# Kernel tuning notes

Measured on AMD Instinct MI355X. Metric: run time of the kernel, lower is better.

The kernel has to match this reference:

```python
import jax, jax.numpy as jnp
import numpy as np

# dimensions
B, NQ, D, H, L, KT, KF = 4, 8192, 256, 8, 4, 2, 2
K = KT * KF
DH = D // H
SPATIAL = np.array([[64, 64], [32, 32], [16, 16], [8, 8]], dtype=np.int32)  # (H_l, W_l)
_sizes = SPATIAL[:, 0] * SPATIAL[:, 1]
LSI = np.concatenate([[0], np.cumsum(_sizes)[:-1]]).astype(np.int32)
NV = int(_sizes.sum())


def setup_inputs() -> dict:
    key = jax.random.key(0)
    ks = jax.random.split(key, 12)
    s = 0.02  # small weight scale keeps tanh in linear region like the zero-init original
    # biases per _reset_parameters: +-0.5 grid for offsets, level-specialization for level_weights
    b_time = jnp.asarray(np.tile(np.linspace(-0.5, 0.5, KT), H * L).astype(np.float32))
    b_freq = jnp.asarray(np.tile(np.linspace(-0.5, 0.5, KF).astype(np.float32), H * L))
    lvl_bias = np.zeros((H, L), dtype=np.float32)
    hpl = max(1, H // L)
    for lvl in range(L):
        lvl_bias[lvl * hpl:min(lvl * hpl + hpl, H), lvl] = 1.0
    return dict(
        query=jax.random.normal(ks[0], (B, NQ, D), jnp.float32),
        reference_points=jax.random.uniform(ks[1], (B, NQ, L, 2), jnp.float32),
        value=jax.random.normal(ks[2], (B, NV, D), jnp.float32),
        spatial_shapes=jnp.asarray(SPATIAL),
        level_start_index=jnp.asarray(LSI),
        W_time=jax.random.normal(ks[3], (D, H * L * KT), jnp.float32) * s,
        b_time=b_time,
        W_freq=jax.random.normal(ks[4], (D, H * L * KF), jnp.float32) * s,
        b_freq=b_freq,
        W_lvl=jax.random.normal(ks[5], (D, H * L), jnp.float32) * s,
        b_lvl=jnp.asarray(lvl_bias.reshape(-1)),
        W_pt=jax.random.normal(ks[6], (D, H * L * K), jnp.float32) * s,
        b_pt=jnp.zeros((H * L * K,), jnp.float32),
        W_v=jax.random.normal(ks[7], (D, D), jnp.float32) * (1.0 / np.sqrt(D)),
        b_v=jnp.zeros((D,), jnp.float32),
        W_o=jax.random.normal(ks[8], (D, D), jnp.float32) * (1.0 / np.sqrt(D)),
        b_o=jnp.zeros((D,), jnp.float32),
    )


def _bilinear(vlev, gx, gy, Hl, Wl):
    # vlev: [B,H,Hl*Wl,DH]; gx,gy: [B,H,NQ,K] normalized grid coords in [-1,1]
    # F.grid_sample(align_corners=False, padding_mode='zeros') semantics
    x = (gx + 1.0) * (Wl * 0.5) - 0.5
    y = (gy + 1.0) * (Hl * 0.5) - 0.5
    x0 = jnp.floor(x)
    y0 = jnp.floor(y)
    wx1 = x - x0
    wy1 = y - y0
    x0i = x0.astype(jnp.int32)
    y0i = y0.astype(jnp.int32)

    def gather(xi, yi, w):
        valid = (xi >= 0) & (xi < Wl) & (yi >= 0) & (yi < Hl)
        idx = jnp.clip(yi, 0, Hl - 1) * Wl + jnp.clip(xi, 0, Wl - 1)
        b, h, nq, k = idx.shape
        v = jnp.take_along_axis(vlev, idx.reshape(b, h, nq * k)[..., None], axis=2)
        v = v.reshape(b, h, nq, k, DH)
        return v * (w * valid)[..., None]

    return (gather(x0i, y0i, (1.0 - wx1) * (1.0 - wy1))
            + gather(x0i + 1, y0i, wx1 * (1.0 - wy1))
            + gather(x0i, y0i + 1, (1.0 - wx1) * wy1)
            + gather(x0i + 1, y0i + 1, wx1 * wy1))


def _forward(query, reference_points, value, W_time, b_time, W_freq, b_freq,
             W_lvl, b_lvl, W_pt, b_pt, W_v, b_v, W_o, b_o,
             spatial_shapes, level_start_index):
    ss = np.asarray(spatial_shapes)
    lsi = np.asarray(level_start_index)
    # predicted separable offsets (offset_scale = 1.0)
    t_off = jnp.tanh(query @ W_time + b_time).reshape(B, NQ, H, L, KT)
    f_off = jnp.tanh(query @ W_freq + b_freq).reshape(B, NQ, H, L, KF)
    # square grid: outer product of time (x) and freq (y) offsets -> K = KT*KF points
    off = jnp.stack([
        jnp.broadcast_to(t_off[..., :, None], (B, NQ, H, L, KT, KF)),
        jnp.broadcast_to(f_off[..., None, :], (B, NQ, H, L, KT, KF)),
    ], axis=-1).reshape(B, NQ, H, L, K, 2)
    # normalizer: (W_l, H_l) per level
    norm = jnp.stack([spatial_shapes[:, 1], spatial_shapes[:, 0]], axis=-1).astype(jnp.float32)
    loc = reference_points[:, :, None, :, None, :] + off / norm[None, None, None, :, None, :]
    loc = jnp.clip(loc, 0.0, 1.0)
    grid = 2.0 * loc - 1.0  # [B,NQ,H,L,K,2], last dim = (x, y)
    # attention weights: softmax over levels times softmax over points
    lw = jax.nn.softmax((query @ W_lvl + b_lvl).reshape(B, NQ, H, L), axis=-1)
    pw = jax.nn.softmax((query @ W_pt + b_pt).reshape(B, NQ, H, L, K), axis=-1)
    attn = lw[..., None] * pw  # [B,NQ,H,L,K]
    v = (value @ W_v + b_v).reshape(B, NV, H, DH)
    out = jnp.zeros((B, NQ, H, DH), jnp.float32)
    for lid in range(L):
        Hl, Wl = int(ss[lid, 0]), int(ss[lid, 1])
        start = int(lsi[lid])
        vlev = v[:, start:start + Hl * Wl].transpose(0, 2, 1, 3)  # [B,H,S_l,DH]
        gx = grid[:, :, :, lid, :, 0].transpose(0, 2, 1, 3)  # [B,H,NQ,K]
        gy = grid[:, :, :, lid, :, 1].transpose(0, 2, 1, 3)
        sampled = _bilinear(vlev, gx, gy, Hl, Wl)  # [B,H,NQ,K,DH]
        a = attn[:, :, :, lid, :].transpose(0, 2, 1, 3)  # [B,H,NQ,K]
        out = out + jnp.einsum('bhqkd,bhqk->bqhd', sampled, a)
    out = out.reshape(B, NQ, D)
    return out @ W_o + b_o


def reference(query, reference_points, value, spatial_shapes, level_start_index,
              W_time, b_time, W_freq, b_freq, W_lvl, b_lvl, W_pt, b_pt,
              W_v, b_v, W_o, b_o):
    return _forward(query, reference_points, value, W_time, b_time, W_freq, b_freq,
                    W_lvl, b_lvl, W_pt, b_pt, W_v, b_v, W_o, b_o,
                    spatial_shapes, level_start_index)
```

## Files before the change

### kernel.cpp

```cpp
#include <hip/hip_runtime.h>
#include <math.h>

#define B_  4
#define NQ_ 8192
#define D_  256
#define H_  8
#define L_  4
#define K_  4
#define DH_ 32
#define NV_ 5440

#define SLAB_ 5936

typedef short bf16x8 __attribute__((ext_vector_type(8)));
typedef float f32x4  __attribute__((ext_vector_type(4)));
typedef float f32x8  __attribute__((ext_vector_type(8)));
typedef unsigned short u16x8 __attribute__((ext_vector_type(8)));

__device__ __forceinline__ ushort f2bf(float f) {
    union { float f; unsigned u; } v; v.f = f;
    return (ushort)((v.u + 0x7FFF + ((v.u >> 16) & 1)) >> 16);
}
__device__ __forceinline__ float bf2f(ushort u) {
    union { unsigned u; float f; } v; v.u = ((unsigned)u) << 16;
    return v.f;
}
__device__ __forceinline__ void gld16(const void* g, void* l) {
    __builtin_amdgcn_global_load_lds(
        (const __attribute__((address_space(1))) unsigned int*)g,
        (__attribute__((address_space(3))) unsigned int*)l, 16, 0, 0);
}

__global__ __launch_bounds__(256) void k_prep(const float* __restrict__ Wv,
                                              const float* __restrict__ Wo,
                                              const float* __restrict__ Wt,
                                              const float* __restrict__ Wf,
                                              const float* __restrict__ Wlv,
                                              const float* __restrict__ Wp,
                                              ushort* __restrict__ Wvt,
                                              ushort* __restrict__ Wot,
                                              ushort* __restrict__ Wqt) {
    const int bk = blockIdx.x;
    const int t  = threadIdx.x;
    if (bk < 512) {
        const float* in; ushort* out; int n;
        if (bk < 256) { in = Wv; out = Wvt; n = bk; }
        else          { in = Wo; out = Wot; n = bk - 256; }
        out[n * 256 + t] = f2bf(in[t * 256 + n]);
    } else {
        const int n = bk - 512;
        float v;
        if (n < 64)       v = Wt[t * 64 + n];
        else if (n < 128) v = Wf[t * 64 + (n - 64)];
        else if (n < 160) v = Wlv[t * 32 + (n - 128)];
        else              v = Wp[t * 128 + (n - 160)];
        Wqt[n * 256 + t] = f2bf(v);
    }
}

__device__ __forceinline__ void vproj_role(char* smem, int fid,
                                           const float* __restrict__ value,
                                           const ushort* __restrict__ Wvt,
                                           const float* __restrict__ bv,
                                           ushort* __restrict__ vperm) {
    ushort* As0 = (ushort*)smem;
    ushort* Bs0 = (ushort*)(smem + 16384);
    const int m0   = (fid % 170) * 128;
    const int n0   = (fid / 170) * 128;
    const int t    = threadIdx.x;
    const int w    = t >> 6;
    const int lane = t & 63;
    const int wm   = (w >> 1) * 64;
    const int wn   = (w & 1) * 64;
    const int lm   = lane & 15;
    const int quad = lane >> 4;

    float4 areg[4];

    auto stageB = [&](int buf, int kc) {
        ushort* B = Bs0 + buf * 4096;
        #pragma unroll
        for (int i = 0; i < 2; ++i) {
            const int c0 = (i * 4 + w) * 64;
            const int c  = c0 + lane;
            const int row = c >> 2, ko = (c & 3) * 8;
            gld16(&Wvt[(size_t)(n0 + row) * 256 + kc + ko], B + (size_t)c0 * 8);
        }
    };
    auto loadA = [&](int kc) {
        #pragma unroll
        for (int i = 0; i < 4; ++i) {
            const int c = t + i * 256;
            const int row = c >> 3, ko = (c & 7) * 4;
            areg[i] = *(const float4*)&value[(size_t)(m0 + row) * 256 + kc + ko];
        }
    };
    auto writeA = [&](int buf) {
        ushort* A = As0 + buf * 4096;
        #pragma unroll
        for (int i = 0; i < 4; ++i) {
            const int c = t + i * 256;
            const int row = c >> 3, ko = (c & 7) * 4;
            ushort4 u;
            u.x = f2bf(areg[i].x); u.y = f2bf(areg[i].y);
            u.z = f2bf(areg[i].z); u.w = f2bf(areg[i].w);
            *(ushort4*)&A[row * 32 + ko] = u;
        }
    };

    f32x4 acc[4][4];
    #pragma unroll
    for (int i = 0; i < 4; ++i)
        #pragma unroll
        for (int j = 0; j < 4; ++j)
            acc[i][j] = (f32x4)(0.f);

    loadA(0); writeA(0);
    stageB(0, 0);
    __syncthreads();

    int cur = 0;
    for (int kc = 0; kc < 256; kc += 32) {
        const int nxt = cur ^ 1;
        const ushort* Ac = As0 + cur * 4096;
        const ushort* Bc = Bs0 + cur * 4096;
        bf16x8 af[4], bfr[4];
        #pragma unroll
        for (int mf = 0; mf < 4; ++mf)
            af[mf] = *(const bf16x8*)&Ac[(wm + mf * 16 + lm) * 32 + quad * 8];
        #pragma unroll
        for (int nf = 0; nf < 4; ++nf)
            bfr[nf] = *(const bf16x8*)&Bc[(wn + nf * 16 + lm) * 32 + quad * 8];
        if (kc + 32 < 256) {
            loadA(kc + 32);
            stageB(nxt, kc + 32);
        }
        #pragma unroll
        for (int mf = 0; mf < 4; ++mf)
            #pragma unroll
            for (int nf = 0; nf < 4; ++nf)
                acc[mf][nf] = __builtin_amdgcn_mfma_f32_16x16x32_bf16(
                    af[mf], bfr[nf], acc[mf][nf], 0, 0, 0);
        if (kc + 32 < 256) {
            writeA(nxt);
            __syncthreads();
        }
        cur = nxt;
    }

    #pragma unroll
    for (int mf = 0; mf < 4; ++mf) {
        #pragma unroll
        for (int nf = 0; nf < 4; ++nf) {
            const f32x4 a = acc[mf][nf];
            const int col   = n0 + wn + nf * 16 + lm;
            const int rbase = m0 + wm + mf * 16 + quad * 4;
            #pragma unroll
            for (int r = 0; r < 4; ++r) {
                const int row = rbase + r;
                const float v = a[r];
                const int b = row / NV_, s = row - b * NV_;
                const int h = col >> 5, dh = col & 31;
                const int l = (s >= 5376) ? 3 : (s >= 5120) ? 2 : (s >= 4096) ? 1 : 0;
                const int lsi_[4] = {0, 4096, 5120, 5376};
                const int po_[4]  = {0, 4356, 5512, 5836};
                const int o  = s - lsi_[l];
                const int Wl = 64 >> l;
                const int y  = o >> (6 - l);
                const int x  = o & (Wl - 1);
                const int prow = po_[l] + (y + 1) * (Wl + 2) + (x + 1);
                vperm[(((size_t)(b * H_ + h)) * SLAB_ + prow) * 32 + dh] =
                    f2bf(v + bv[col]);
            }
        }
    }
}

__device__ __forceinline__ void qproj_role(char* smem, int fid,
                                           const float* __restrict__ query,
                                           const ushort* __restrict__ Wqt,
                                           const float* __restrict__ refpts,
                                           const float* __restrict__ bt,
                                           const float* __restrict__ bfq,
                                           const float* __restrict__ blv,
                                           const float* __restrict__ bp,
                                           float* __restrict__ params) {
    ushort* As0 = (ushort*)smem;
    ushort* Bs0 = (ushort*)(smem + 8192);
    float*  ep  = (float*)smem;

    const int m0   = fid * 64;
    const int t    = threadIdx.x;
    const int w    = t >> 6;
    const int lane = t & 63;
    const int wm   = (w >> 1) * 32;
    const int wn   = (w & 1) * 144;
    const int lm   = lane & 15;
    const int quad = lane >> 4;

    float4 areg[2];

    auto stageB = [&](int buf, int kc) {
        ushort* B = Bs0 + buf * 9216;
        #pragma unroll
        for (int i = 0; i < 5; ++i) {
            const int cb = i * 4 + w;
            if (cb < 18) {
                const int c0 = cb * 64;
                const int c  = c0 + lane;
                const int row = c >> 2, ko = (c & 3) * 8;
                gld16(&Wqt[(size_t)row * 256 + kc + ko], B + (size_t)c0 * 8);
            }
        }
    };
    auto loadA = [&](int kc) {
        #pragma unroll
        for (int i = 0; i < 2; ++i) {
            const int c = t + i * 256;
            const int row = c >> 3, ko = (c & 7) * 4;
            areg[i] = *(const float4*)&query[(size_t)(m0 + row) * 256 + kc + ko];
        }
    };
    auto writeA = [&](int buf) {
        ushort* A = As0 + buf * 2048;
        #pragma unroll
        for (int i = 0; i < 2; ++i) {
            const int c = t + i * 256;
            const int row = c >> 3, ko = (c & 7) * 4;
            ushort4 u;
            u.x = f2bf(areg[i].x); u.y = f2bf(areg[i].y);
            u.z = f2bf(areg[i].z); u.w = f2bf(areg[i].w);
            *(ushort4*)&A[row * 32 + ko] = u;
        }
    };

    f32x4 acc[2][9];
    #pragma unroll
    for (int i = 0; i < 2; ++i)
        #pragma unroll
        for (int j = 0; j < 9; ++j)
            acc[i][j] = (f32x4)(0.f);

    loadA(0); writeA(0);
    stageB(0, 0);
    __syncthreads();

    int cur = 0;
    for (int kc = 0; kc < 256; kc += 32) {
        const int nxt = cur ^ 1;
        const ushort* Ac = As0 + cur * 2048;
        const ushort* Bc = Bs0 + cur * 9216;
        bf16x8 af[2], bfr[9];
        #pragma unroll
        for (int mf = 0; mf < 2; ++mf)
            af[mf] = *(const bf16x8*)&Ac[(wm + mf * 16 + lm) * 32 + quad * 8];
        #pragma unroll
        for (int nf = 0; nf < 9; ++nf)
            bfr[nf] = *(const bf16x8*)&Bc[(wn + nf * 16 + lm) * 32 + quad * 8];
        if (kc + 32 < 256) {
            loadA(kc + 32);
            stageB(nxt, kc + 32);
        }
        #pragma unroll
        for (int mf = 0; mf < 2; ++mf)
            #pragma unroll
            for (int nf = 0; nf < 9; ++nf)
                acc[mf][nf] = __builtin_amdgcn_mfma_f32_16x16x32_bf16(
                    af[mf], bfr[nf], acc[mf][nf], 0, 0, 0);
        if (kc + 32 < 256) {
            writeA(nxt);
            __syncthreads();
        }
        cur = nxt;
    }

    #pragma unroll
    for (int ph = 0; ph < 2; ++ph) {
        __syncthreads();
        if ((w >> 1) == ph) {
            #pragma unroll
            for (int mf = 0; mf < 2; ++mf)
                #pragma unroll
                for (int nf = 0; nf < 9; ++nf)
                    #pragma unroll
                    for (int r = 0; r < 4; ++r)
                        ep[(mf * 16 + quad * 4 + r) * 296 + wn + nf * 16 + lm]
                            = acc[mf][nf][r];
        }
        __syncthreads();
        #pragma unroll
        for (int it = 0; it < 4; ++it) {
            const int item = t + it * 256;
            const int qr = item >> 5;
            const int hl = item & 31;
            const int h = hl >> 2, l = hl & 3;
            const int qg = m0 + ph * 32 + qr;
            const float* lgr = &ep[qr * 296];

            const float tA = tanhf(lgr[hl * 2 + 0] + bt[hl * 2 + 0]);
            const float tB = tanhf(lgr[hl * 2 + 1] + bt[hl * 2 + 1]);
            const float fA = tanhf(lgr[64 + hl * 2 + 0] + bfq[hl * 2 + 0]);
            const float fB = tanhf(lgr[64 + hl * 2 + 1] + bfq[hl * 2 + 1]);

            const float l0 = lgr[128 + h * 4 + 0] + blv[h * 4 + 0];
            const float l1 = lgr[128 + h * 4 + 1] + blv[h * 4 + 1];
            const float l2 = lgr[128 + h * 4 + 2] + blv[h * 4 + 2];
            const float l3 = lgr[128 + h * 4 + 3] + blv[h * 4 + 3];
            const float lmx = fmaxf(fmaxf(l0, l1), fmaxf(l2, l3));
            const float e0 = __expf(l0 - lmx), e1 = __expf(l1 - lmx);
            const float e2 = __expf(l2 - lmx), e3 = __expf(l3 - lmx);
            const float lsum = e0 + e1 + e2 + e3;
            const float lwv = ((l == 0) ? e0 : (l == 1) ? e1 : (l == 2) ? e2 : e3) / lsum;

            const float p0 = lgr[160 + hl * 4 + 0] + bp[hl * 4 + 0];
            const float p1 = lgr[160 + hl * 4 + 1] + bp[hl * 4 + 1];
            const float p2 = lgr[160 + hl * 4 + 2] + bp[hl * 4 + 2];
            const float p3 = lgr[160 + hl * 4 + 3] + bp[hl * 4 + 3];
            const float pmx = fmaxf(fmaxf(p0, p1), fmaxf(p2, p3));
            const float q0e = __expf(p0 - pmx), q1e = __expf(p1 - pmx);
            const float q2e = __expf(p2 - pmx), q3e = __expf(p3 - pmx);
            const float inv = lwv / (q0e + q1e + q2e + q3e);

            const float rx = refpts[((size_t)qg * L_ + l) * 2 + 0];
            const float ry = refpts[((size_t)qg * L_ + l) * 2 + 1];
            const float Wlf = (float)(64 >> l);
            const float Hlf = (float)(64 >> l);
            const float xA = fminf(fmaxf(rx + tA / Wlf, 0.f), 1.f) * Wlf - 0.5f;
            const float xB = fminf(fmaxf(rx + tB / Wlf, 0.f), 1.f) * Wlf - 0.5f;
            const float yA = fminf(fmaxf(ry + fA / Hlf, 0.f), 1.f) * Hlf - 0.5f;
            const float yB = fminf(fmaxf(ry + fB / Hlf, 0.f), 1.f) * Hlf - 0.5f;

            float* pp = params + (size_t)qg * 256 + hl * 8;
            pp[0] = q0e * inv; pp[1] = q1e * inv; pp[2] = q2e * inv; pp[3] = q3e * inv;
            pp[4] = xA; pp[5] = xB; pp[6] = yA; pp[7] = yB;
        }
    }
}

__device__ __forceinline__ void border_role(int fid, ushort* __restrict__ vperm) {
    const int t = threadIdx.x;
    const int p = fid * 256 + t;
    const int bh = p / 496;
    int e = p - bh * 496;
    int l = 0;
    if (e >= 460)      { l = 3; e -= 460; }
    else if (e >= 392) { l = 2; e -= 392; }
    else if (e >= 260) { l = 1; e -= 260; }
    const int po_[4] = {0, 4356, 5512, 5836};
    const int W2 = (64 >> l) + 2;
    int row, col;
    if (e < 2 * W2) {
        row = (e < W2) ? 0 : (W2 - 1);
        col = (e < W2) ? e : (e - W2);
    } else {
        const int e2 = e - 2 * W2;
        row = 1 + (e2 >> 1);
        col = (e2 & 1) ? (W2 - 1) : 0;
    }
    uint4* dst = (uint4*)&vperm[((size_t)bh * SLAB_ + po_[l] + row * W2 + col) * 32];
    dst[0] = make_uint4(0, 0, 0, 0);
    dst[1] = make_uint4(0, 0, 0, 0);
    dst[2] = make_uint4(0, 0, 0, 0);
    dst[3] = make_uint4(0, 0, 0, 0);
}

__global__ __launch_bounds__(256) void k_fused(const float* __restrict__ value,
                                               const ushort* __restrict__ Wvt,
                                               const float* __restrict__ bv,
                                               ushort* __restrict__ vperm,
                                               const float* __restrict__ query,
                                               const ushort* __restrict__ Wqt,
                                               const float* __restrict__ refpts,
                                               const float* __restrict__ bt,
                                               const float* __restrict__ bfq,
                                               const float* __restrict__ blv,
                                               const float* __restrict__ bp,
                                               float* __restrict__ params) {
    __shared__ __align__(16) char smem[45056];
    const int fid = blockIdx.x;
    if (fid < 340) {
        vproj_role(smem, fid, value, Wvt, bv, vperm);
    } else if (fid < 852) {
        qproj_role(smem, fid - 340, query, Wqt, refpts, bt, bfq, blv, bp, params);
    } else {
        border_role(fid - 852, vperm);
    }
}

__global__ __launch_bounds__(256) void k_ogemm(const ushort* __restrict__ A,
                                               const ushort* __restrict__ Bt,
                                               const float* __restrict__ bias,
                                               float* __restrict__ Cp) {
    __shared__ __align__(16) ushort As[2][128 * 32];
    __shared__ __align__(16) ushort Bs[2][128 * 32];
    const int m0   = blockIdx.x * 128;
    const int n0   = blockIdx.y * 128;
    const int t    = threadIdx.x;
    const int w    = t >> 6;
    const int lane = t & 63;
    const int wm   = (w >> 1) * 64;
    const int wn   = (w & 1) * 64;
    const int lm   = lane & 15;
    const int quad = lane >> 4;

    auto stage = [&](ushort* dst, const ushort* src, int row0, int kc) {
        #pragma unroll
        for (int i = 0; i < 2; ++i) {
            const int c0 = (i * 4 + w) * 64;
            const int c  = c0 + lane;
            const int row = c >> 2, ko = (c & 3) * 8;
            gld16(&src[(size_t)(row0 + row) * 256 + kc + ko], dst + (size_t)c0 * 8);
        }
    };

    f32x4 acc[4][4];
    #pragma unroll
    for (int i = 0; i < 4; ++i)
        #pragma unroll
        for (int j = 0; j < 4; ++j)
            acc[i][j] = (f32x4)(0.f);

    stage(&As[0][0], A, m0, 0);
    stage(&Bs[0][0], Bt, n0, 0);
    __syncthreads();

    int cur = 0;
    for (int kc = 0; kc < 256; kc += 32) {
        const int nxt = cur ^ 1;
        bf16x8 af[4], bfr[4];
        #pragma unroll
        for (int mf = 0; mf < 4; ++mf)
            af[mf] = *(const bf16x8*)&As[cur][(wm + mf * 16 + lm) * 32 + quad * 8];
        #pragma unroll
        for (int nf = 0; nf < 4; ++nf)
            bfr[nf] = *(const bf16x8*)&Bs[cur][(wn + nf * 16 + lm) * 32 + quad * 8];
        if (kc + 32 < 256) {
            stage(&As[nxt][0], A, m0, kc + 32);
            stage(&Bs[nxt][0], Bt, n0, kc + 32);
        }
        #pragma unroll
        for (int mf = 0; mf < 4; ++mf)
            #pragma unroll
            for (int nf = 0; nf < 4; ++nf)
                acc[mf][nf] = __builtin_amdgcn_mfma_f32_16x16x32_bf16(
                    af[mf], bfr[nf], acc[mf][nf], 0, 0, 0);
        if (kc + 32 < 256) __syncthreads();
        cur = nxt;
    }

    #pragma unroll
    for (int mf = 0; mf < 4; ++mf) {
        #pragma unroll
        for (int nf = 0; nf < 4; ++nf) {
            const f32x4 a = acc[mf][nf];
            const int col   = n0 + wn + nf * 16 + lm;
            const int rbase = m0 + wm + mf * 16 + quad * 4;
            #pragma unroll
            for (int r = 0; r < 4; ++r)
                Cp[(size_t)(rbase + r) * 256 + col] = a[r] + bias[col];
        }
    }
}

__global__ __launch_bounds__(256) void k_sample(const ushort* __restrict__ vperm,
                                                const float* __restrict__ params,
                                                ushort* __restrict__ mid) {
    __shared__ float pm[8][264];
    const int fid = blockIdx.x;
    const int b   = (fid & 7) >> 1;
    const int q0  = (((fid >> 3) << 1) | (fid & 1)) * 8;
    const int t   = threadIdx.x;
    const int ql  = t >> 5;
    const int sub = t & 31;
    const int h   = sub >> 2;
    const int dh8 = sub & 3;

    for (int i = t; i < 8 * 256; i += 256) {
        const int q = i >> 8, c = i & 255;
        pm[q][(c >> 5) * 33 + (c & 31)] = params[((size_t)(b * NQ_ + q0 + q)) * 256 + c];
    }
    __syncthreads();

    const ushort* vb = vperm + ((size_t)(b * H_ + h)) * SLAB_ * 32 + dh8 * 8;
    const int po_[4] = {0, 4356, 5512, 5836};

    f32x8 acc = (f32x8)(0.f);
    #pragma unroll
    for (int l = 0; l < L_; ++l) {
        const int W2 = (64 >> l) + 2;
        const ushort* vl = vb + (size_t)po_[l] * 32;
        const float* p  = &pm[ql][h * 33 + l * 8];
        const float a0 = p[0], a1 = p[1], a2 = p[2], a3 = p[3];
        const float xA = p[4], xB = p[5], yA = p[6], yB = p[7];
        const float xa0 = floorf(xA), xb0 = floorf(xB);
        const float ya0 = floorf(yA), yb0 = floorf(yB);
        const float fxa = xA - xa0, fxb = xB - xb0;
        const float fya = yA - ya0, fyb = yB - yb0;
        const int pxa = (int)xa0 + 1, pxb = (int)xb0 + 1;
        const int pya = (int)ya0 + 1, pyb = (int)yb0 + 1;
        #pragma unroll
        for (int k = 0; k < 4; ++k) {
            const int   px = (k & 2) ? pxb : pxa;
            const int   py = (k & 1) ? pyb : pya;
            const float fx = (k & 2) ? fxb : fxa;
            const float fy = (k & 1) ? fyb : fya;
            const float ak = (k == 0) ? a0 : (k == 1) ? a1 : (k == 2) ? a2 : a3;
            const ushort* cp = vl + (size_t)(py * W2 + px) * 32;
            const u16x8 u00 = *(const u16x8*)cp;
            const u16x8 u10 = *(const u16x8*)(cp + 32);
            const u16x8 u01 = *(const u16x8*)(cp + W2 * 32);
            const u16x8 u11 = *(const u16x8*)(cp + (W2 + 1) * 32);
            const float gx = 1.f - fx, gy = 1.f - fy;
            const float w00 = ak * gx * gy, w10 = ak * fx * gy;
            const float w01 = ak * gx * fy, w11 = ak * fx * fy;
            #pragma unroll
            for (int e = 0; e < 8; ++e)
                acc[e] += bf2f(u00[e]) * w00 + bf2f(u10[e]) * w10
                        + bf2f(u01[e]) * w01 + bf2f(u11[e]) * w11;
        }
    }
    u16x8 o;
    #pragma unroll
    for (int e = 0; e < 8; ++e) o[e] = f2bf(acc[e]);
    *(u16x8*)&mid[((size_t)(b * NQ_ + q0 + ql)) * 256 + sub * 8] = o;
}

extern "C" void kernel_launch(void* const* d_in, const int* in_sizes, int n_in,
                              void* d_out, int out_size, void* d_ws, size_t ws_size,
                              hipStream_t stream) {
    const float* query = (const float*)d_in[0];
    const float* refp  = (const float*)d_in[1];
    const float* value = (const float*)d_in[2];
    const float* Wt = (const float*)d_in[5];
    const float* bt = (const float*)d_in[6];
    const float* Wf = (const float*)d_in[7];
    const float* bf = (const float*)d_in[8];
    const float* Wl = (const float*)d_in[9];
    const float* bl = (const float*)d_in[10];
    const float* Wp = (const float*)d_in[11];
    const float* bp = (const float*)d_in[12];
    const float* Wv = (const float*)d_in[13];
    const float* bv = (const float*)d_in[14];
    const float* Wo = (const float*)d_in[15];
    const float* bo = (const float*)d_in[16];

    char* wsb = (char*)d_ws;
    ushort* vperm  = (ushort*)wsb;
    float*  params = (float*)(wsb + 12156928);
    ushort* midb   = (ushort*)(wsb + 45711360);
    ushort* Wvt    = (ushort*)(wsb + 62488576);
    ushort* Wot    = (ushort*)(wsb + 62619648);
    ushort* Wqt    = (ushort*)(wsb + 62750720);

    k_prep<<<800, 256, 0, stream>>>(Wv, Wo, Wt, Wf, Wl, Wp, Wvt, Wot, Wqt);
    k_fused<<<914, 256, 0, stream>>>(value, Wvt, bv, vperm,
                                     query, Wqt, refp, bt, bf, bl, bp, params);
    k_sample<<<dim3(NQ_ / 8 * B_), 256, 0, stream>>>(vperm, params, midb);
    k_ogemm<<<dim3(256, 2), 256, 0, stream>>>(midb, Wot, bo, (float*)d_out);
}
```

Baseline: 220.8 us.

## Fuse bilinear sampling with the output projection GEMM in one kernel

Merges the sampling kernel and the output-projection GEMM into one 512-thread kernel. Each block samples 16 queries into a bf16 tile in shared memory, then multiplies that tile by the full Wo matrix with MFMA, streaming Wo through double-buffered shared memory. This removes the intermediate bf16 buffer write and read plus one kernel launch. In exchange every block re-reads the whole 128 KB Wo, the 16-row MFMA tiles are small, and the larger shared-memory footprint may lower occupancy.

```diff
diff --git a/kernel.cpp b/kernel.cpp
--- a/kernel.cpp
+++ b/kernel.cpp
@@ -387,95 +387,25 @@
     }
 }
 
-__global__ __launch_bounds__(256) void k_ogemm(const ushort* __restrict__ A,
-                                               const ushort* __restrict__ Bt,
-                                               const float* __restrict__ bias,
-                                               float* __restrict__ Cp) {
-    __shared__ __align__(16) ushort As[2][128 * 32];
-    __shared__ __align__(16) ushort Bs[2][128 * 32];
-    const int m0   = blockIdx.x * 128;
-    const int n0   = blockIdx.y * 128;
-    const int t    = threadIdx.x;
-    const int w    = t >> 6;
-    const int lane = t & 63;
-    const int wm   = (w >> 1) * 64;
-    const int wn   = (w & 1) * 64;
-    const int lm   = lane & 15;
-    const int quad = lane >> 4;
-
-    auto stage = [&](ushort* dst, const ushort* src, int row0, int kc) {
-        #pragma unroll
-        for (int i = 0; i < 2; ++i) {
-            const int c0 = (i * 4 + w) * 64;
-            const int c  = c0 + lane;
-            const int row = c >> 2, ko = (c & 3) * 8;
-            gld16(&src[(size_t)(row0 + row) * 256 + kc + ko], dst + (size_t)c0 * 8);
-        }
-    };
-
-    f32x4 acc[4][4];
-    #pragma unroll
-    for (int i = 0; i < 4; ++i)
-        #pragma unroll
-        for (int j = 0; j < 4; ++j)
-            acc[i][j] = (f32x4)(0.f);
-
-    stage(&As[0][0], A, m0, 0);
-    stage(&Bs[0][0], Bt, n0, 0);
-    __syncthreads();
-
-    int cur = 0;
-    for (int kc = 0; kc < 256; kc += 32) {
-        const int nxt = cur ^ 1;
-        bf16x8 af[4], bfr[4];
-        #pragma unroll
-        for (int mf = 0; mf < 4; ++mf)
-            af[mf] = *(const bf16x8*)&As[cur][(wm + mf * 16 + lm) * 32 + quad * 8];
-        #pragma unroll
-        for (int nf = 0; nf < 4; ++nf)
-            bfr[nf] = *(const bf16x8*)&Bs[cur][(wn + nf * 16 + lm) * 32 + quad * 8];
-        if (kc + 32 < 256) {
-            stage(&As[nxt][0], A, m0, kc + 32);
-            stage(&Bs[nxt][0], Bt, n0, kc + 32);
-        }
-        #pragma unroll
-        for (int mf = 0; mf < 4; ++mf)
-            #pragma unroll
-            for (int nf = 0; nf < 4; ++nf)
-                acc[mf][nf] = __builtin_amdgcn_mfma_f32_16x16x32_bf16(
-                    af[mf], bfr[nf], acc[mf][nf], 0, 0, 0);
-        if (kc + 32 < 256) __syncthreads();
-        cur = nxt;
-    }
-
-    #pragma unroll
-    for (int mf = 0; mf < 4; ++mf) {
-        #pragma unroll
-        for (int nf = 0; nf < 4; ++nf) {
-            const f32x4 a = acc[mf][nf];
-            const int col   = n0 + wn + nf * 16 + lm;
-            const int rbase = m0 + wm + mf * 16 + quad * 4;
-            #pragma unroll
-            for (int r = 0; r < 4; ++r)
-                Cp[(size_t)(rbase + r) * 256 + col] = a[r] + bias[col];
-        }
-    }
-}
-
-__global__ __launch_bounds__(256) void k_sample(const ushort* __restrict__ vperm,
-                                                const float* __restrict__ params,
-                                                ushort* __restrict__ mid) {
-    __shared__ float pm[8][264];
+#define SST_ 264
+__global__ __launch_bounds__(512) void k_samp(const ushort* __restrict__ vperm,
+                                              const float* __restrict__ params,
+                                              const ushort* __restrict__ Wot,
+                                              const float* __restrict__ bo,
+                                              float* __restrict__ outp) {
+    __shared__ float  pm[16][264];
+    __shared__ __align__(16) ushort S[16 * SST_];
+    __shared__ __align__(16) ushort Bs[2][256 * 32];
     const int fid = blockIdx.x;
     const int b   = (fid & 7) >> 1;
-    const int q0  = (((fid >> 3) << 1) | (fid & 1)) * 8;
+    const int q0  = (((fid >> 3) << 1) | (fid & 1)) * 16;
     const int t   = threadIdx.x;
     const int ql  = t >> 5;
     const int sub = t & 31;
     const int h   = sub >> 2;
     const int dh8 = sub & 3;
 
-    for (int i = t; i < 8 * 256; i += 256) {
+    for (int i = t; i < 16 * 256; i += 512) {
         const int q = i >> 8, c = i & 255;
         pm[q][(c >> 5) * 33 + (c & 31)] = params[((size_t)(b * NQ_ + q0 + q)) * 256 + c];
     }
@@ -522,7 +452,59 @@
     u16x8 o;
     #pragma unroll
     for (int e = 0; e < 8; ++e) o[e] = f2bf(acc[e]);
-    *(u16x8*)&mid[((size_t)(b * NQ_ + q0 + ql)) * 256 + sub * 8] = o;
+    *(u16x8*)&S[ql * SST_ + sub * 8] = o;
+
+    const int w    = t >> 6;
+    const int lane = t & 63;
+    const int lm   = lane & 15;
+    const int quad = lane >> 4;
+    const int wn   = w * 32;
+
+    auto stageB = [&](int buf, int kc) {
+        #pragma unroll
+        for (int i = 0; i < 2; ++i) {
+            const int c0 = (i * 8 + w) * 64;
+            const int c  = c0 + lane;
+            const int row = c >> 2, ko = (c & 3) * 8;
+            gld16(&Wot[(size_t)row * 256 + kc + ko],
+                  (ushort*)&Bs[buf][0] + (size_t)c0 * 8);
+        }
+    };
+
+    f32x4 oacc[2];
+    oacc[0] = (f32x4)(0.f);
+    oacc[1] = (f32x4)(0.f);
+
+    stageB(0, 0);
+    __syncthreads();
+
+    int cur = 0;
+    for (int kc = 0; kc < 256; kc += 32) {
+        const int nxt = cur ^ 1;
+        const bf16x8 af = *(const bf16x8*)&S[lm * SST_ + kc + quad * 8];
+        bf16x8 bfr[2];
+        #pragma unroll
+        for (int nf = 0; nf < 2; ++nf)
+            bfr[nf] = *(const bf16x8*)&Bs[cur][(wn + nf * 16 + lm) * 32 + quad * 8];
+        if (kc + 32 < 256) stageB(nxt, kc + 32);
+        #pragma unroll
+        for (int nf = 0; nf < 2; ++nf)
+            oacc[nf] = __builtin_amdgcn_mfma_f32_16x16x32_bf16(
+                af, bfr[nf], oacc[nf], 0, 0, 0);
+        if (kc + 32 < 256) __syncthreads();
+        cur = nxt;
+    }
+
+    #pragma unroll
+    for (int nf = 0; nf < 2; ++nf) {
+        const int col = wn + nf * 16 + lm;
+        const float bb = bo[col];
+        #pragma unroll
+        for (int r = 0; r < 4; ++r) {
+            const int qr = quad * 4 + r;
+            outp[((size_t)(b * NQ_ + q0 + qr)) * 256 + col] = oacc[nf][r] + bb;
+        }
+    }
 }
 
 extern "C" void kernel_launch(void* const* d_in, const int* in_sizes, int n_in,
@@ -547,7 +529,6 @@
     char* wsb = (char*)d_ws;
     ushort* vperm  = (ushort*)wsb;
     float*  params = (float*)(wsb + 12156928);
-    ushort* midb   = (ushort*)(wsb + 45711360);
     ushort* Wvt    = (ushort*)(wsb + 62488576);
     ushort* Wot    = (ushort*)(wsb + 62619648);
     ushort* Wqt    = (ushort*)(wsb + 62750720);
@@ -555,6 +536,5 @@
     k_prep<<<800, 256, 0, stream>>>(Wv, Wo, Wt, Wf, Wl, Wp, Wvt, Wot, Wqt);
     k_fused<<<914, 256, 0, stream>>>(value, Wvt, bv, vperm,
                                      query, Wqt, refp, bt, bf, bl, bp, params);
-    k_sample<<<dim3(NQ_ / 8 * B_), 256, 0, stream>>>(vperm, params, midb);
-    k_ogemm<<<dim3(256, 2), 256, 0, stream>>>(midb, Wot, bo, (float*)d_out);
-}
+    k_samp<<<2048, 512, 0, stream>>>(vperm, params, Wot, bo, (float*)d_out);
+}
```

Result: slower. 235.9 us (+6.8%).
